# Kernel tuning notes

Measured on AMD Instinct MI355X. Metric: run time of the kernel, lower is better.

## Reference

```python
import jax, jax.numpy as jnp
import numpy as np

N = 4096      # num utterances (graph nodes)
D = 512       # utt_embed_size * 2
W = 10        # att_window_size
S = 8         # num speakers
WIN = 2 * W + 1


def setup_inputs() -> dict:
    key = jax.random.key(0)
    ks = jax.random.split(key, 7)
    s = 0.05  # keep activations in a sane range through two layers
    return {
        "context_embeds": jax.random.normal(ks[0], (N, D), jnp.float32),
        "speakers": jax.random.randint(ks[1], (N,), 0, S),
        "w_gc1": jax.random.normal(ks[2], (4, D, D), jnp.float32) * s,
        "w_gc2": jax.random.normal(ks[3], (4, D, D), jnp.float32) * s,
        "w_att": jax.random.normal(ks[4], (D, D), jnp.float32) * s,
        "w_aggr1": jax.random.normal(ks[5], (D, D), jnp.float32) * s,
        "w_aggr2": jax.random.normal(ks[6], (D, D), jnp.float32) * s,
    }


def _relation_adjs(x, speakers, w_att):
    """Windowed edge attention + 4 relation-masked adjacency matrices."""
    n = x.shape[0]
    pad = jnp.zeros((W, D), x.dtype)
    padded = jnp.concatenate([pad, x, pad], axis=0)          # [n+2W, D]
    # banded gather: row j sees padded[j : j+2W+1]  == cols j-W .. j+W
    gidx = jnp.arange(n)[:, None] + jnp.arange(WIN)[None, :]
    fat = padded[gidx]
    raw = jnp.einsum('nwd,ed->nwe', fat, w_att)               # Linear: x @ W^T
    scores = jnp.einsum('nwe,ne->nw', raw, x)
    attn = jax.nn.softmax(scores, axis=1)                     # softmax over full window (pads included, as original)
    # scatter attention into a banded [n, n] mask
    cols = jnp.arange(n)[:, None] + jnp.arange(WIN)[None, :] - W
    valid = (cols >= 0) & (cols < n)
    rows = jnp.broadcast_to(jnp.arange(n)[:, None], cols.shape)
    attn_mask = jnp.zeros((n, n), x.dtype).at[
        rows, jnp.clip(cols, 0, n - 1)].add(jnp.where(valid, attn, 0.0))
    i = jnp.arange(n)[:, None]
    j = jnp.arange(n)[None, :]
    band = jnp.abs(j - i) <= W
    same_spk = speakers[:, None] == speakers[None, :]
    pred = ((j >= i) & band).astype(x.dtype) * attn_mask      # successors-in-time kept (triu) within window
    suc = ((j < i) & band).astype(x.dtype) * attn_mask        # strict past within window
    same = (same_spk & band).astype(x.dtype) * attn_mask
    diff = ((~same_spk) & band).astype(x.dtype) * attn_mask
    return jnp.stack([pred, suc, same, diff])                 # [4, n, n]


def _gcn_layer(h, adjs, w_gc, w_aggr):
    # sum_r  A_r @ (h @ W_r)  + h @ W_aggr, then relu
    hw = jnp.einsum('md,rde->rme', h, w_gc)                   # [4, n, D]
    agg = jnp.einsum('rnm,rme->ne', adjs, hw)                 # [n, D]
    return jax.nn.relu(agg + h @ w_aggr)


def reference(context_embeds, speakers, w_gc1, w_gc2, w_att, w_aggr1, w_aggr2):
    adjs = _relation_adjs(context_embeds, speakers, w_att)
    h1 = _gcn_layer(context_embeds, adjs, w_gc1, w_aggr1)
    h2 = _gcn_layer(h1, adjs, w_gc2, w_aggr2)
    return h2
```

## Files before the change

### kernel.cpp

```cpp
#include <hip/hip_runtime.h>


#define NN 4096

typedef __bf16 bf16x8 __attribute__((ext_vector_type(8)));
typedef float f32x4 __attribute__((ext_vector_type(4)));
typedef unsigned short u16;
typedef unsigned int u32;

__device__ __forceinline__ u16 f2bf(float f) {
  unsigned u = __float_as_uint(f);
  unsigned r = u + 0x7FFFu + ((u >> 16) & 1u);
  return (u16)(r >> 16);
}
__device__ __forceinline__ float bf2f(u16 h) {
  return __uint_as_float(((unsigned)h) << 16);
}
__device__ __forceinline__ float blo(u32 v) { return __uint_as_float(v << 16); }
__device__ __forceinline__ float bhi(u32 v) { return __uint_as_float(v & 0xffff0000u); }
__device__ __forceinline__ u32 packbf(float a, float b) {
  return (u32)f2bf(a) | ((u32)f2bf(b) << 16);
}

__device__ __forceinline__ void gload_lds16(const u16* g, u16* l) {
  __builtin_amdgcn_global_load_lds(
      (const __attribute__((address_space(1))) void*)g,
      (__attribute__((address_space(3))) void*)l, 16, 0, 0);
}

__global__ __launch_bounds__(256) void prep_t(const float* __restrict__ w_att,
                                              const float* __restrict__ w_gc1,
                                              const float* __restrict__ w_aggr1,
                                              const float* __restrict__ w_gc2,
                                              const float* __restrict__ w_aggr2,
                                              u16* __restrict__ Batt,
                                              u16* __restrict__ Wt1, u16* __restrict__ Wt2) {
  __shared__ float t[64][65];
  const int b = blockIdx.x, tid = threadIdx.x;
  const int r = tid >> 6, c = tid & 63;
  if (b < 512) {
    const int lay = b >> 8, tb = b & 255;
    const int jt = tb >> 3, kt = tb & 7;
    const float* g = lay ? w_gc2 : w_gc1;
    const float* wa = lay ? w_aggr2 : w_aggr1;
    u16* Wt = lay ? Wt2 : Wt1;
    const int p = (jt * 64) >> 9;
    const int jj0 = (jt * 64) & 511;
    const int k0 = kt * 64;
#pragma unroll
    for (int i = 0; i < 16; ++i) {
      int rr = r + i * 4;
      size_t o = (size_t)(k0 + rr) * 512 + jj0 + c;
      float v;
      if (p == 0)      v = g[o] - g[262144 + o];
      else if (p == 1) v = g[524288 + o] - g[786432 + o];
      else if (p == 2) v = g[262144 + o] + g[786432 + o];
      else             v = wa[o];
      t[c][rr] = v;
    }
    __syncthreads();
#pragma unroll
    for (int i = 0; i < 16; ++i) {
      int jl = r + i * 4;
      Wt[(size_t)(jt * 64 + jl) * 512 + k0 + c] = f2bf(t[jl][c]);
    }
  } else {
    const int tb = b - 512;
    const int et = tb >> 3, jt2 = tb & 7;
    const int e0 = et * 64, j0 = jt2 * 64;
#pragma unroll
    for (int i = 0; i < 16; ++i) {
      int rr = r + i * 4;
      t[c][rr] = w_att[(size_t)(e0 + rr) * 512 + j0 + c];
    }
    __syncthreads();
#pragma unroll
    for (int i = 0; i < 16; ++i) {
      int jl = r + i * 4;
      float v = t[jl][c];
      u16 hi = f2bf(v), lo = f2bf(v - bf2f(hi));
      u16* row = Batt + (size_t)(j0 + jl) * 1536;
      row[e0 + c] = hi;
      row[512 + e0 + c] = hi;
      row[1024 + e0 + c] = lo;
    }
  }
}

__global__ __launch_bounds__(256) void prep_main(const float* __restrict__ x,
                                                 const int* __restrict__ spk,
                                                 u16* __restrict__ Aatt,
                                                 float* __restrict__ xp,
                                                 u32* __restrict__ xWg,
                                                 u32* __restrict__ h1Wg,
                                                 int* __restrict__ spkp) {
  const int tid = threadIdx.x;
  for (int vb = blockIdx.x; vb < 8529; vb += 2048) {
    if (vb < 8192) {
      int s = vb >> 3;
      int r = 512 * (vb & 7) + (s >> 1);
      int c = ((s & 1) << 8) + tid;
      float v = x[(size_t)r * 512 + c];
      u16 hi = f2bf(v), lo = f2bf(v - bf2f(hi));
      u16* row = Aatt + (size_t)r * 1536;
      row[c] = hi; row[512 + c] = lo; row[1024 + c] = hi;
      xp[(size_t)(r + 16) * 512 + c] = v;
    } else if (vb < 8256) {
      int idx = (vb - 8192) * 256 + tid;
      int g = idx >> 9, c = idx & 511;
      int row = (g < 16) ? g : 4112 + (g - 16);
      xp[(size_t)row * 512 + c] = 0.f;
    } else if (vb < 8384) {
      int idx = (vb - 8256) * 256 + tid;
      int g = idx >> 10, c = idx & 1023;
      int row = (g < 16) ? g : 4112 + (g - 16);
      xWg[(size_t)row * 1024 + c] = 0;
    } else if (vb < 8512) {
      int idx = (vb - 8384) * 256 + tid;
      int g = idx >> 10, c = idx & 1023;
      int row = (g < 16) ? g : 4112 + (g - 16);
      h1Wg[(size_t)row * 1024 + c] = 0;
    } else {
      int idx = (vb - 8512) * 256 + tid;
      if (idx < 4128)
        spkp[idx] = (idx >= 16 && idx < 4112) ? spk[idx - 16] : -9;
    }
  }
}

__device__ __forceinline__ void xcd_align(int gx, int& bx, int& by) {
  int lid = by * gx + bx;
  int xcd = lid & 7;
  int s = lid >> 3;
  int q = s / gx;
  bx = s - q * gx;
  by = xcd * 4 + q;
}

__device__ __forceinline__ void gemm_core(const u16* __restrict__ A, const u16* __restrict__ Bt,
                                          int K, int lda, int ldb, size_t bm, size_t bn,
                                          u16 (&As)[2][8192], u16 (&Bs)[2][8192],
                                          f32x4 (&acc)[4][4]) {
  const int tid = threadIdx.x;
  const int lane = tid & 63;
  const int wave = tid >> 6;
  const int wr = wave >> 1, wc = wave & 1;
  const int arow = wr * 64 + (lane & 15);
  const int bcol = wc * 64 + (lane & 15);
  const int nt = K >> 6;

  auto STAGE = [&](int t, int bi) {
    const int k0 = t << 6;
#pragma unroll
    for (int c4 = 0; c4 < 4; ++c4) {
      const int o = (c4 * 256 + tid) * 16;
      const int r = o >> 7;
      const int sc = (((o >> 4) & 7) ^ (r & 7)) << 3;
      gload_lds16(A + (bm + r) * lda + k0 + sc, &As[bi][o >> 1]);
      gload_lds16(Bt + (bn + r) * ldb + k0 + sc, &Bs[bi][o >> 1]);
    }
  };

  STAGE(0, 0);
  for (int t = 0; t < nt; ++t) {
    const int cur = t & 1;
    if (t + 1 < nt) {
      STAGE(t + 1, cur ^ 1);
      asm volatile("s_waitcnt vmcnt(8)" ::: "memory");
    } else {
      asm volatile("s_waitcnt vmcnt(0)" ::: "memory");
    }
    __builtin_amdgcn_s_barrier();
    asm volatile("" ::: "memory");
    bf16x8 af[4][2], bfr[4][2];
#pragma unroll
    for (int i = 0; i < 4; ++i)
#pragma unroll
      for (int ks = 0; ks < 2; ++ks) {
        const int ar = arow + i * 16;
        const int ac = ((ks * 4 + (lane >> 4)) ^ (ar & 7)) << 4;
        af[i][ks] = *(const bf16x8*)((const char*)&As[cur][0] + ar * 128 + ac);
        const int br = bcol + i * 16;
        const int bc = ((ks * 4 + (lane >> 4)) ^ (br & 7)) << 4;
        bfr[i][ks] = *(const bf16x8*)((const char*)&Bs[cur][0] + br * 128 + bc);
      }
#pragma unroll
    for (int ks = 0; ks < 2; ++ks)
#pragma unroll
      for (int i = 0; i < 4; ++i)
#pragma unroll
        for (int j = 0; j < 4; ++j)
          acc[i][j] = __builtin_amdgcn_mfma_f32_16x16x32_bf16(af[i][ks], bfr[j][ks],
                                                              acc[i][j], 0, 0, 0);
    asm volatile("s_waitcnt lgkmcnt(0)" ::: "memory");
    __builtin_amdgcn_sched_barrier(0);
    __builtin_amdgcn_s_barrier();
  }
}

__global__ __launch_bounds__(256, 2) void fat_gemm(const u16* __restrict__ Aatt,
                                                   const u16* __restrict__ Wt1,
                                                   const u16* __restrict__ Batt,
                                                   u16* __restrict__ xW, float* __restrict__ y) {
  __shared__ u16 As[2][8192];
  __shared__ u16 Bs[2][8192];
  f32x4 acc[4][4] = {};
  const int tid = threadIdx.x;
  const int lane = tid & 63;
  const int wave = tid >> 6;
  const int wr = wave >> 1, wc = wave & 1;
  int bx = blockIdx.x, by = blockIdx.y;
  xcd_align(28, bx, by);
  const size_t bm = (size_t)by * 128;
  const bool yp = bx < 12;
  const int kp = yp ? (bx >> 2) : 0;
  const size_t bn = yp ? (size_t)(bx & 3) * 128 : (size_t)(bx - 12) * 128;

  if (yp)
    gemm_core(Aatt + kp * 512, Batt + kp * 512, 512, 1536, 1536, bm, bn, As, Bs, acc);
  else
    gemm_core(Aatt, Wt1, 512, 1536, 512, bm, bn, As, Bs, acc);

  const size_t crow = bm + wr * 64 + ((lane >> 4) * 4);
  const size_t ccol = bn + wc * 64 + (lane & 15);
  float* yk = y + (size_t)kp * NN * 512;
#pragma unroll
  for (int i = 0; i < 4; ++i)
#pragma unroll
    for (int j = 0; j < 4; ++j)
#pragma unroll
      for (int b = 0; b < 4; ++b) {
        size_t r = crow + i * 16 + b, c = ccol + j * 16;
        if (yp)
          yk[r * 512 + c] = acc[i][j][b];
        else
          xW[r * 2048 + c] = f2bf(acc[i][j][b]);
      }
}

__global__ __launch_bounds__(256, 2) void gemm_l2(const u16* __restrict__ h1,
                                                  const u16* __restrict__ Wt2,
                                                  u16* __restrict__ h1W) {
  __shared__ u16 As[2][8192];
  __shared__ u16 Bs[2][8192];
  f32x4 acc[4][4] = {};
  const int tid = threadIdx.x;
  const int lane = tid & 63;
  const int wave = tid >> 6;
  const int wr = wave >> 1, wc = wave & 1;
  int bx = blockIdx.x, by = blockIdx.y;
  xcd_align(16, bx, by);
  const size_t bm = (size_t)by * 128;
  const size_t bn = (size_t)bx * 128;
  gemm_core(h1, Wt2, 512, 512, 512, bm, bn, As, Bs, acc);
  const size_t crow = bm + wr * 64 + ((lane >> 4) * 4);
  const size_t ccol = bn + wc * 64 + (lane & 15);
#pragma unroll
  for (int i = 0; i < 4; ++i)
#pragma unroll
    for (int j = 0; j < 4; ++j)
#pragma unroll
      for (int b = 0; b < 4; ++b) {
        size_t r = crow + i * 16 + b, c = ccol + j * 16;
        h1W[r * 2048 + c] = f2bf(acc[i][j][b]);
      }
}

__device__ __forceinline__ int xcd_row(int b) { return (b & 7) * 512 + (b >> 3); }

__global__ void gather1(const float* __restrict__ xp, const float* __restrict__ y,
                        const u16* __restrict__ xW, const int* __restrict__ spkp,
                        float* __restrict__ attn, u16* __restrict__ h1) {
  const int n = xcd_row(blockIdx.x);
  const int tid = threadIdx.x;
  __shared__ float ys[512];
  __shared__ float sc[21];
  __shared__ float av[21], apv[21], asv[21];
  __shared__ int sps[21];
  const int mysp = spkp[16 + n];
  {
    const float* y0 = y + (size_t)n * 512;
    const float* y1 = y0 + (size_t)NN * 512;
    const float* y2 = y1 + (size_t)NN * 512;
    ys[tid] = y0[tid] + y1[tid] + y2[tid];
    ys[tid + 256] = y0[tid + 256] + y1[tid + 256] + y2[tid + 256];
  }
  if (tid < 21) sps[tid] = spkp[16 + n - 10 + tid];
  __syncthreads();
  const int wave = tid >> 6, lane = tid & 63;
  for (int w = wave; w < 21; w += 4) {
    const float* xm = xp + (size_t)(n + 6 + w) * 512;
    float p = 0.f;
#pragma unroll
    for (int i = 0; i < 8; ++i) p += xm[lane + i * 64] * ys[lane + i * 64];
#pragma unroll
    for (int off = 32; off; off >>= 1) p += __shfl_xor(p, off, 64);
    if (lane == 0) sc[w] = p;
  }
  __syncthreads();
  if (tid < 64) {
    float v = (tid < 21) ? sc[tid] : -1e30f;
    float mx = v;
#pragma unroll
    for (int off = 32; off; off >>= 1) mx = fmaxf(mx, __shfl_xor(mx, off, 64));
    float e = (tid < 21) ? __expf(v - mx) : 0.f;
    float sum = e;
#pragma unroll
    for (int off = 32; off; off >>= 1) sum += __shfl_xor(sum, off, 64);
    if (tid < 21) {
      int m = n + tid - 10;
      float a = (0 <= m && m < NN) ? (e / sum) : 0.f;
      av[tid] = a;
      apv[tid] = (tid >= 10) ? a : 0.f;
      asv[tid] = (sps[tid] == mysp) ? a : 0.f;
      attn[(size_t)n * 24 + tid] = a;
    }
  }
  __syncthreads();
  const u32* xW32 = (const u32*)xW;
  u32 hv = xW32[(size_t)n * 1024 + 768 + tid];
  float a0 = blo(hv), a1 = bhi(hv);
#pragma unroll
  for (int w = 0; w < 10; ++w) {
    const u32* row = xW32 + (ptrdiff_t)(n - 10 + w) * 1024 + tid;
    u32 vs = row[256], va = row[512];
    float s2 = asv[w], a = av[w];
    a0 += s2 * blo(vs) + a * blo(va);
    a1 += s2 * bhi(vs) + a * bhi(va);
  }
#pragma unroll
  for (int w = 10; w < 21; ++w) {
    const u32* row = xW32 + (ptrdiff_t)(n - 10 + w) * 1024 + tid;
    u32 vp = row[0], vs = row[256], va = row[512];
    float ap = apv[w], s2 = asv[w], a = av[w];
    a0 += ap * blo(vp) + s2 * blo(vs) + a * blo(va);
    a1 += ap * bhi(vp) + s2 * bhi(vs) + a * bhi(va);
  }
  ((u32*)(h1 + (size_t)n * 512))[tid] = packbf(fmaxf(a0, 0.f), fmaxf(a1, 0.f));
}

__global__ void gather2(const u16* __restrict__ h1W, const float* __restrict__ attn,
                        const int* __restrict__ spkp, float* __restrict__ out) {
  const int n = xcd_row(blockIdx.x);
  const int tid = threadIdx.x;
  __shared__ float av[21], apv[21], asv[21];
  if (tid < 21) {
    float a = attn[(size_t)n * 24 + tid];
    int sp = spkp[16 + n - 10 + tid];
    av[tid] = a;
    apv[tid] = (tid >= 10) ? a : 0.f;
    asv[tid] = (sp == spkp[16 + n]) ? a : 0.f;
  }
  __syncthreads();
  const u32* hW32 = (const u32*)h1W;
  u32 hv = hW32[(size_t)n * 1024 + 768 + tid];
  float a0 = blo(hv), a1 = bhi(hv);
#pragma unroll
  for (int w = 0; w < 10; ++w) {
    const u32* row = hW32 + (ptrdiff_t)(n - 10 + w) * 1024 + tid;
    u32 vs = row[256], va = row[512];
    float s2 = asv[w], a = av[w];
    a0 += s2 * blo(vs) + a * blo(va);
    a1 += s2 * bhi(vs) + a * bhi(va);
  }
#pragma unroll
  for (int w = 10; w < 21; ++w) {
    const u32* row = hW32 + (ptrdiff_t)(n - 10 + w) * 1024 + tid;
    u32 vp = row[0], vs = row[256], va = row[512];
    float ap = apv[w], s2 = asv[w], a = av[w];
    a0 += ap * blo(vp) + s2 * blo(vs) + a * blo(va);
    a1 += ap * bhi(vp) + s2 * bhi(vs) + a * bhi(va);
  }
  float* o = out + (size_t)n * 512 + tid * 2;
  o[0] = fmaxf(a0, 0.f);
  o[1] = fmaxf(a1, 0.f);
}

extern "C" void kernel_launch(void* const* d_in, const int* in_sizes, int n_in,
                              void* d_out, int out_size, void* d_ws, size_t ws_size,
                              hipStream_t stream) {
  const float* x = (const float*)d_in[0];
  const int* spk = (const int*)d_in[1];
  const float* w_gc1 = (const float*)d_in[2];
  const float* w_gc2 = (const float*)d_in[3];
  const float* w_att = (const float*)d_in[4];
  const float* w_aggr1 = (const float*)d_in[5];
  const float* w_aggr2 = (const float*)d_in[6];

  char* p = (char*)d_ws;
  u16* Aatt = (u16*)p;  p += (size_t)NN * 1536 * 2;
  u16* Batt = (u16*)p;  p += (size_t)512 * 1536 * 2;
  u16* Wt1 = (u16*)p;   p += (size_t)2048 * 512 * 2;
  u16* Wt2 = (u16*)p;   p += (size_t)2048 * 512 * 2;
  float* xp = (float*)p; p += (size_t)4128 * 512 * 4;
  float* y = (float*)p; p += (size_t)3 * NN * 512 * 4;
  float* attn = (float*)p; p += (size_t)NN * 24 * 4;
  u16* xWg = (u16*)p;   p += (size_t)4128 * 2048 * 2;
  u16* h1 = (u16*)p;    p += (size_t)NN * 512 * 2;
  u16* h1Wg = (u16*)p;  p += (size_t)4128 * 2048 * 2;
  int* spkp = (int*)p;  p += (size_t)4128 * 4;

  u16* xW = xWg + (size_t)16 * 2048;
  u16* h1W = h1Wg + (size_t)16 * 2048;

  prep_t<<<576, 256, 0, stream>>>(w_att, w_gc1, w_aggr1, w_gc2, w_aggr2, Batt, Wt1, Wt2);

  prep_main<<<2048, 256, 0, stream>>>(x, spk, Aatt, xp, (u32*)xWg, (u32*)h1Wg, spkp);

  fat_gemm<<<dim3(28, 32), 256, 0, stream>>>(Aatt, Wt1, Batt, xW, y);

  gather1<<<NN, 256, 0, stream>>>(xp, y, xW, spkp, attn, h1);

  gemm_l2<<<dim3(16, 32), 256, 0, stream>>>(h1, Wt2, h1W);

  gather2<<<NN, 256, 0, stream>>>(h1W, attn, spkp, (float*)d_out);
}
```

Before: 91.88 us.

## Interleave relation outputs for vector gathers, fuse prep kernels, restructure GEMM pipeline

GEMM epilogues now write the four per-relation projection columns interleaved, so each gather thread loads one 16-byte vector per window row instead of three or four scattered 4-byte loads. The two prep kernels are merged into one launch. The GEMM main loop now waits for all loads, synchronises, and only then issues the next stage's prefetch, replacing the partial vmcnt wait. The scattered 2-byte epilogue stores and the weaker load/compute overlap in the GEMM may add cost.

```diff
diff --git a/kernel.cpp b/kernel.cpp
--- a/kernel.cpp
+++ b/kernel.cpp
@@ -28,74 +28,72 @@
       (__attribute__((address_space(3))) void*)l, 16, 0, 0);
 }
 
-__global__ __launch_bounds__(256) void prep_t(const float* __restrict__ w_att,
-                                              const float* __restrict__ w_gc1,
-                                              const float* __restrict__ w_aggr1,
-                                              const float* __restrict__ w_gc2,
-                                              const float* __restrict__ w_aggr2,
-                                              u16* __restrict__ Batt,
-                                              u16* __restrict__ Wt1, u16* __restrict__ Wt2) {
+__device__ __forceinline__ int ileave(int j) {
+  int p = j >> 9, cc = j & 511;
+  return (cc >> 1) * 8 + p * 2 + (cc & 1);
+}
+
+__global__ __launch_bounds__(256) void prep_fused(
+    const float* __restrict__ x, const float* __restrict__ w_att,
+    const float* __restrict__ w_gc1, const float* __restrict__ w_aggr1,
+    const float* __restrict__ w_gc2, const float* __restrict__ w_aggr2,
+    const int* __restrict__ spk, u16* __restrict__ Aatt, u16* __restrict__ Batt,
+    u16* __restrict__ Wt1, u16* __restrict__ Wt2, float* __restrict__ xp,
+    u32* __restrict__ xWg, u32* __restrict__ h1Wg, int* __restrict__ spkp) {
   __shared__ float t[64][65];
   const int b = blockIdx.x, tid = threadIdx.x;
-  const int r = tid >> 6, c = tid & 63;
-  if (b < 512) {
-    const int lay = b >> 8, tb = b & 255;
-    const int jt = tb >> 3, kt = tb & 7;
-    const float* g = lay ? w_gc2 : w_gc1;
-    const float* wa = lay ? w_aggr2 : w_aggr1;
-    u16* Wt = lay ? Wt2 : Wt1;
-    const int p = (jt * 64) >> 9;
-    const int jj0 = (jt * 64) & 511;
-    const int k0 = kt * 64;
-#pragma unroll
-    for (int i = 0; i < 16; ++i) {
-      int rr = r + i * 4;
-      size_t o = (size_t)(k0 + rr) * 512 + jj0 + c;
-      float v;
-      if (p == 0)      v = g[o] - g[262144 + o];
-      else if (p == 1) v = g[524288 + o] - g[786432 + o];
-      else if (p == 2) v = g[262144 + o] + g[786432 + o];
-      else             v = wa[o];
-      t[c][rr] = v;
+  if (b < 576) {
+    const int r = tid >> 6, c = tid & 63;
+    if (b < 512) {
+      const int lay = b >> 8, tb = b & 255;
+      const int jt = tb >> 3, kt = tb & 7;
+      const float* g = lay ? w_gc2 : w_gc1;
+      const float* wa = lay ? w_aggr2 : w_aggr1;
+      u16* Wt = lay ? Wt2 : Wt1;
+      const int p = (jt * 64) >> 9;
+      const int jj0 = (jt * 64) & 511;
+      const int k0 = kt * 64;
+#pragma unroll
+      for (int i = 0; i < 16; ++i) {
+        int rr = r + i * 4;
+        size_t o = (size_t)(k0 + rr) * 512 + jj0 + c;
+        float v;
+        if (p == 0)      v = g[o] - g[262144 + o];
+        else if (p == 1) v = g[524288 + o] - g[786432 + o];
+        else if (p == 2) v = g[262144 + o] + g[786432 + o];
+        else             v = wa[o];
+        t[c][rr] = v;
+      }
+      __syncthreads();
+#pragma unroll
+      for (int i = 0; i < 16; ++i) {
+        int jl = r + i * 4;
+        Wt[(size_t)(jt * 64 + jl) * 512 + k0 + c] = f2bf(t[jl][c]);
+      }
+    } else {
+      const int tb = b - 512;
+      const int et = tb >> 3, jt2 = tb & 7;
+      const int e0 = et * 64, j0 = jt2 * 64;
+#pragma unroll
+      for (int i = 0; i < 16; ++i) {
+        int rr = r + i * 4;
+        t[c][rr] = w_att[(size_t)(e0 + rr) * 512 + j0 + c];
+      }
+      __syncthreads();
+#pragma unroll
+      for (int i = 0; i < 16; ++i) {
+        int jl = r + i * 4;
+        float v = t[jl][c];
+        u16 hi = f2bf(v), lo = f2bf(v - bf2f(hi));
+        u16* row = Batt + (size_t)(j0 + jl) * 1536;
+        row[e0 + c] = hi;
+        row[512 + e0 + c] = hi;
+        row[1024 + e0 + c] = lo;
+      }
     }
-    __syncthreads();
-#pragma unroll
-    for (int i = 0; i < 16; ++i) {
-      int jl = r + i * 4;
-      Wt[(size_t)(jt * 64 + jl) * 512 + k0 + c] = f2bf(t[jl][c]);
-    }
-  } else {
-    const int tb = b - 512;
-    const int et = tb >> 3, jt2 = tb & 7;
-    const int e0 = et * 64, j0 = jt2 * 64;
-#pragma unroll
-    for (int i = 0; i < 16; ++i) {
-      int rr = r + i * 4;
-      t[c][rr] = w_att[(size_t)(e0 + rr) * 512 + j0 + c];
-    }
-    __syncthreads();
-#pragma unroll
-    for (int i = 0; i < 16; ++i) {
-      int jl = r + i * 4;
-      float v = t[jl][c];
-      u16 hi = f2bf(v), lo = f2bf(v - bf2f(hi));
-      u16* row = Batt + (size_t)(j0 + jl) * 1536;
-      row[e0 + c] = hi;
-      row[512 + e0 + c] = hi;
-      row[1024 + e0 + c] = lo;
-    }
-  }
-}
-
-__global__ __launch_bounds__(256) void prep_main(const float* __restrict__ x,
-                                                 const int* __restrict__ spk,
-                                                 u16* __restrict__ Aatt,
-                                                 float* __restrict__ xp,
-                                                 u32* __restrict__ xWg,
-                                                 u32* __restrict__ h1Wg,
-                                                 int* __restrict__ spkp) {
-  const int tid = threadIdx.x;
-  for (int vb = blockIdx.x; vb < 8529; vb += 2048) {
+    return;
+  }
+  for (int vb = b - 576; vb < 8529; vb += 2048) {
     if (vb < 8192) {
       int s = vb >> 3;
       int r = 512 * (vb & 7) + (s >> 1);
@@ -164,14 +162,10 @@
   STAGE(0, 0);
   for (int t = 0; t < nt; ++t) {
     const int cur = t & 1;
-    if (t + 1 < nt) {
-      STAGE(t + 1, cur ^ 1);
-      asm volatile("s_waitcnt vmcnt(8)" ::: "memory");
-    } else {
-      asm volatile("s_waitcnt vmcnt(0)" ::: "memory");
-    }
+    asm volatile("s_waitcnt vmcnt(0) lgkmcnt(0)" ::: "memory");
+    __builtin_amdgcn_sched_barrier(0);
     __builtin_amdgcn_s_barrier();
-    asm volatile("" ::: "memory");
+    if (t + 1 < nt) STAGE(t + 1, cur ^ 1);
     bf16x8 af[4][2], bfr[4][2];
 #pragma unroll
     for (int i = 0; i < 4; ++i)
@@ -192,10 +186,8 @@
         for (int j = 0; j < 4; ++j)
           acc[i][j] = __builtin_amdgcn_mfma_f32_16x16x32_bf16(af[i][ks], bfr[j][ks],
                                                               acc[i][j], 0, 0, 0);
-    asm volatile("s_waitcnt lgkmcnt(0)" ::: "memory");
-    __builtin_amdgcn_sched_barrier(0);
-    __builtin_amdgcn_s_barrier();
-  }
+  }
+  asm volatile("s_waitcnt lgkmcnt(0)" ::: "memory");
 }
 
 __global__ __launch_bounds__(256, 2) void fat_gemm(const u16* __restrict__ Aatt,
@@ -230,11 +222,12 @@
     for (int j = 0; j < 4; ++j)
 #pragma unroll
       for (int b = 0; b < 4; ++b) {
-        size_t r = crow + i * 16 + b, c = ccol + j * 16;
+        size_t r = crow + i * 16 + b;
+        int c = (int)ccol + j * 16;
         if (yp)
           yk[r * 512 + c] = acc[i][j][b];
         else
-          xW[r * 2048 + c] = f2bf(acc[i][j][b]);
+          xW[r * 2048 + ileave(c)] = f2bf(acc[i][j][b]);
       }
 }
 
@@ -261,15 +254,16 @@
     for (int j = 0; j < 4; ++j)
 #pragma unroll
       for (int b = 0; b < 4; ++b) {
-        size_t r = crow + i * 16 + b, c = ccol + j * 16;
-        h1W[r * 2048 + c] = f2bf(acc[i][j][b]);
+        size_t r = crow + i * 16 + b;
+        int c = (int)ccol + j * 16;
+        h1W[r * 2048 + ileave(c)] = f2bf(acc[i][j][b]);
       }
 }
 
 __device__ __forceinline__ int xcd_row(int b) { return (b & 7) * 512 + (b >> 3); }
 
 __global__ void gather1(const float* __restrict__ xp, const float* __restrict__ y,
-                        const u16* __restrict__ xW, const int* __restrict__ spkp,
+                        const uint4* __restrict__ xW4, const int* __restrict__ spkp,
                         float* __restrict__ attn, u16* __restrict__ h1) {
   const int n = xcd_row(blockIdx.x);
   const int tid = threadIdx.x;
@@ -317,29 +311,19 @@
     }
   }
   __syncthreads();
-  const u32* xW32 = (const u32*)xW;
-  u32 hv = xW32[(size_t)n * 1024 + 768 + tid];
-  float a0 = blo(hv), a1 = bhi(hv);
-#pragma unroll
-  for (int w = 0; w < 10; ++w) {
-    const u32* row = xW32 + (ptrdiff_t)(n - 10 + w) * 1024 + tid;
-    u32 vs = row[256], va = row[512];
-    float s2 = asv[w], a = av[w];
-    a0 += s2 * blo(vs) + a * blo(va);
-    a1 += s2 * bhi(vs) + a * bhi(va);
-  }
-#pragma unroll
-  for (int w = 10; w < 21; ++w) {
-    const u32* row = xW32 + (ptrdiff_t)(n - 10 + w) * 1024 + tid;
-    u32 vp = row[0], vs = row[256], va = row[512];
+  uint4 sv = xW4[(size_t)n * 256 + tid];
+  float a0 = blo(sv.w), a1 = bhi(sv.w);
+#pragma unroll
+  for (int w = 0; w < 21; ++w) {
+    const uint4 v = xW4[(ptrdiff_t)(n - 10 + w) * 256 + tid];
     float ap = apv[w], s2 = asv[w], a = av[w];
-    a0 += ap * blo(vp) + s2 * blo(vs) + a * blo(va);
-    a1 += ap * bhi(vp) + s2 * bhi(vs) + a * bhi(va);
+    a0 += ap * blo(v.x) + s2 * blo(v.y) + a * blo(v.z);
+    a1 += ap * bhi(v.x) + s2 * bhi(v.y) + a * bhi(v.z);
   }
   ((u32*)(h1 + (size_t)n * 512))[tid] = packbf(fmaxf(a0, 0.f), fmaxf(a1, 0.f));
 }
 
-__global__ void gather2(const u16* __restrict__ h1W, const float* __restrict__ attn,
+__global__ void gather2(const uint4* __restrict__ hW4, const float* __restrict__ attn,
                         const int* __restrict__ spkp, float* __restrict__ out) {
   const int n = xcd_row(blockIdx.x);
   const int tid = threadIdx.x;
@@ -352,24 +336,14 @@
     asv[tid] = (sp == spkp[16 + n]) ? a : 0.f;
   }
   __syncthreads();
-  const u32* hW32 = (const u32*)h1W;
-  u32 hv = hW32[(size_t)n * 1024 + 768 + tid];
-  float a0 = blo(hv), a1 = bhi(hv);
-#pragma unroll
-  for (int w = 0; w < 10; ++w) {
-    const u32* row = hW32 + (ptrdiff_t)(n - 10 + w) * 1024 + tid;
-    u32 vs = row[256], va = row[512];
-    float s2 = asv[w], a = av[w];
-    a0 += s2 * blo(vs) + a * blo(va);
-    a1 += s2 * bhi(vs) + a * bhi(va);
-  }
-#pragma unroll
-  for (int w = 10; w < 21; ++w) {
-    const u32* row = hW32 + (ptrdiff_t)(n - 10 + w) * 1024 + tid;
-    u32 vp = row[0], vs = row[256], va = row[512];
+  uint4 sv = hW4[(size_t)n * 256 + tid];
+  float a0 = blo(sv.w), a1 = bhi(sv.w);
+#pragma unroll
+  for (int w = 0; w < 21; ++w) {
+    const uint4 v = hW4[(ptrdiff_t)(n - 10 + w) * 256 + tid];
     float ap = apv[w], s2 = asv[w], a = av[w];
-    a0 += ap * blo(vp) + s2 * blo(vs) + a * blo(va);
-    a1 += ap * bhi(vp) + s2 * bhi(vs) + a * bhi(va);
+    a0 += ap * blo(v.x) + s2 * blo(v.y) + a * blo(v.z);
+    a1 += ap * bhi(v.x) + s2 * bhi(v.y) + a * bhi(v.z);
   }
   float* o = out + (size_t)n * 512 + tid * 2;
   o[0] = fmaxf(a0, 0.f);
@@ -403,15 +377,15 @@
   u16* xW = xWg + (size_t)16 * 2048;
   u16* h1W = h1Wg + (size_t)16 * 2048;
 
-  prep_t<<<576, 256, 0, stream>>>(w_att, w_gc1, w_aggr1, w_gc2, w_aggr2, Batt, Wt1, Wt2);
-
-  prep_main<<<2048, 256, 0, stream>>>(x, spk, Aatt, xp, (u32*)xWg, (u32*)h1Wg, spkp);
+  prep_fused<<<2624, 256, 0, stream>>>(x, w_att, w_gc1, w_aggr1, w_gc2, w_aggr2, spk,
+                                       Aatt, Batt, Wt1, Wt2, xp, (u32*)xWg, (u32*)h1Wg,
+                                       spkp);
 
   fat_gemm<<<dim3(28, 32), 256, 0, stream>>>(Aatt, Wt1, Batt, xW, y);
 
-  gather1<<<NN, 256, 0, stream>>>(xp, y, xW, spkp, attn, h1);
+  gather1<<<NN, 256, 0, stream>>>(xp, y, (const uint4*)xW, spkp, attn, h1);
 
   gemm_l2<<<dim3(16, 32), 256, 0, stream>>>(h1, Wt2, h1W);
 
-  gather2<<<NN, 256, 0, stream>>>(h1W, attn, spkp, (float*)d_out);
-}
+  gather2<<<NN, 256, 0, stream>>>((const uint4*)h1W, attn, spkp, (float*)d_out);
+}
```

After: 97.93 us. 1.07x slower.
